# Kernel tuning notes

Measured on AMD Instinct MI355X. Metric: run time of the kernel, lower is better.

The kernel has to match this reference:

```python
import jax, jax.numpy as jnp
import numpy as np

B = 8
NUM_CLASSES = 80
STRIDES = (8, 16, 32, 64, 128)
HS = (96, 48, 24, 12, 6)
WS = (160, 80, 40, 20, 10)
IMG_H, IMG_W = 768, 1280
OCTAVE_SCALE = 4.0
LOC_THR = 0.01
SCORE_THR = 0.05
IOU_THR = 0.5
NMS_PRE = 1000
MAX_PER_IMG = 100
MAX_RATIO_ANCHOR = abs(float(np.log(1e-6)))        # anchor_coder wh_ratio_clip=1e-6
MAX_RATIO_BBOX = abs(float(np.log(16.0 / 1000.0)))  # bbox_coder default wh_ratio_clip
CLS_OFFSET = 4096.0  # > max image coord, separates classes for class-aware NMS


def setup_inputs():
    inp = {}
    k = 0
    for i, (h, w) in enumerate(zip(HS, WS)):
        for name, c in (("cls_score", NUM_CLASSES), ("bbox_pred", 4), ("shape_pred", 2), ("loc_pred", 1)):
            k += 1
            inp[f"{name}_{i}"] = jax.random.normal(jax.random.fold_in(jax.random.key(0), k), (B, c, h, w), dtype=jnp.float32)
    return inp


def _squares(h, w, stride):
    # mmdet square anchor generator: base size stride*octave_base_scale, ratio 1, center offset 0
    xs = jnp.arange(w, dtype=jnp.float32) * stride
    ys = jnp.arange(h, dtype=jnp.float32) * stride
    yy, xx = jnp.meshgrid(ys, xs, indexing="ij")
    half = 0.5 * OCTAVE_SCALE * stride
    return jnp.stack([xx - half, yy - half, xx + half, yy + half], -1).reshape(-1, 4)


def _delta2bbox(rois, deltas, max_ratio, max_shape=None):
    dx, dy = deltas[..., 0], deltas[..., 1]
    dw = jnp.clip(deltas[..., 2], -max_ratio, max_ratio)
    dh = jnp.clip(deltas[..., 3], -max_ratio, max_ratio)
    px = (rois[..., 0] + rois[..., 2]) * 0.5
    py = (rois[..., 1] + rois[..., 3]) * 0.5
    pw = rois[..., 2] - rois[..., 0]
    ph = rois[..., 3] - rois[..., 1]
    gx = px + pw * dx
    gy = py + ph * dy
    gw = pw * jnp.exp(dw)
    gh = ph * jnp.exp(dh)
    x1, y1 = gx - 0.5 * gw, gy - 0.5 * gh
    x2, y2 = gx + 0.5 * gw, gy + 0.5 * gh
    if max_shape is not None:
        x1 = jnp.clip(x1, 0.0, float(max_shape[1]))
        x2 = jnp.clip(x2, 0.0, float(max_shape[1]))
        y1 = jnp.clip(y1, 0.0, float(max_shape[0]))
        y2 = jnp.clip(y2, 0.0, float(max_shape[0]))
    return jnp.stack([x1, y1, x2, y2], -1)


def _level(cls, bbox, shp, loc, stride, h, w):
    b = cls.shape[0]
    # NOTE: double sigmoid is faithful to the original wrapper (it sigmoids twice)
    scores = jax.nn.sigmoid(jax.nn.sigmoid(jnp.transpose(cls, (0, 2, 3, 1)).reshape(b, -1, NUM_CLASSES)))
    mask = (jax.nn.sigmoid(loc) >= LOC_THR).astype(scores.dtype)
    mask = jnp.transpose(mask, (0, 2, 3, 1)).reshape(b, -1)  # num_anchors == 1
    scores = scores * mask[:, :, None]
    deltas = jnp.transpose(shp, (0, 2, 3, 1)).reshape(b, -1, 2)
    bdel = jnp.concatenate([jnp.zeros_like(deltas), deltas], axis=-1)  # [0,0,dw,dh]
    anchors = _delta2bbox(_squares(h, w, stride)[None], bdel, MAX_RATIO_ANCHOR)  # guided anchors
    bbox = jnp.transpose(bbox, (0, 2, 3, 1)).reshape(b, -1, 4)
    n = scores.shape[1]
    if n < NMS_PRE:  # pad_with_value
        pad = NMS_PRE - n
        scores = jnp.pad(scores, ((0, 0), (0, pad), (0, 0)))
        bbox = jnp.pad(bbox, ((0, 0), (0, pad), (0, 0)))
        anchors = jnp.pad(anchors, ((0, 0), (0, pad), (0, 0)))
    _, idx = jax.lax.top_k(scores.max(-1), NMS_PRE)
    scores = jnp.take_along_axis(scores, idx[:, :, None], axis=1)
    bbox = jnp.take_along_axis(bbox, idx[:, :, None], axis=1)
    anchors = jnp.take_along_axis(anchors, idx[:, :, None], axis=1)
    proposals = _delta2bbox(anchors, bbox, MAX_RATIO_BBOX, (IMG_H, IMG_W))
    return scores, proposals


def _iou_one_vs_all(box, boxes):
    lt = jnp.maximum(box[:2], boxes[:, :2])
    rb = jnp.minimum(box[2:], boxes[:, 2:])
    wh = jnp.clip(rb - lt, 0.0, None)
    inter = wh[:, 0] * wh[:, 1]
    a1 = (box[2] - box[0]) * (box[3] - box[1])
    a2 = (boxes[:, 2] - boxes[:, 0]) * (boxes[:, 3] - boxes[:, 1])
    return inter / (a1 + a2 - inter + 1e-6)


def _nms_single(scores, boxes):
    # class-aware greedy NMS (BatchedNMS semantics): scores [N,C], boxes [N,4]
    n, c = scores.shape
    s = jnp.where(scores > SCORE_THR, scores, 0.0).reshape(-1)  # [N*C]
    offs = (jnp.arange(c, dtype=boxes.dtype) * CLS_OFFSET)[None, :, None]
    cboxes = (boxes[:, None, :] + offs).reshape(-1, 4)  # class-offset boxes

    def step(sv, _):
        i = jnp.argmax(sv)
        sc = sv[i]
        keep = sc > 0.0
        iou = _iou_one_vs_all(cboxes[i], cboxes)
        sv = jnp.where(iou > IOU_THR, 0.0, sv)  # suppresses i itself too
        cls = jnp.where(keep, (i % c).astype(jnp.int32), -1)
        return sv, (boxes[i // c], sc, cls, keep)

    _, (ob, osc, ocls, okeep) = jax.lax.scan(step, s, None, length=MAX_PER_IMG)
    kf = okeep.astype(boxes.dtype)
    return okeep.sum().astype(jnp.int32), ob * kf[:, None], osc * kf, ocls


def _forward(tensors):
    mlvl_scores, mlvl_props = [], []
    for i in range(5):
        s, p = _level(tensors[4 * i], tensors[4 * i + 1], tensors[4 * i + 2], tensors[4 * i + 3],
                      STRIDES[i], HS[i], WS[i])
        mlvl_scores.append(s)
        mlvl_props.append(p)
    scores = jnp.concatenate(mlvl_scores, axis=1)   # [B, 5000, 80]
    props = jnp.concatenate(mlvl_props, axis=1)     # [B, 5000, 4]
    k = min(max(1000, NMS_PRE), scores.shape[1])
    _, idx = jax.lax.top_k(scores.max(-1), k)
    scores = jnp.take_along_axis(scores, idx[:, :, None], axis=1)
    props = jnp.take_along_axis(props, idx[:, :, None], axis=1)
    return jax.vmap(_nms_single)(scores, props)


def reference(cls_score_0, bbox_pred_0, shape_pred_0, loc_pred_0,
              cls_score_1, bbox_pred_1, shape_pred_1, loc_pred_1,
              cls_score_2, bbox_pred_2, shape_pred_2, loc_pred_2,
              cls_score_3, bbox_pred_3, shape_pred_3, loc_pred_3,
              cls_score_4, bbox_pred_4, shape_pred_4, loc_pred_4):
    tensors = [cls_score_0, bbox_pred_0, shape_pred_0, loc_pred_0,
               cls_score_1, bbox_pred_1, shape_pred_1, loc_pred_1,
               cls_score_2, bbox_pred_2, shape_pred_2, loc_pred_2,
               cls_score_3, bbox_pred_3, shape_pred_3, loc_pred_3,
               cls_score_4, bbox_pred_4, shape_pred_4, loc_pred_4]
    num_detected, proposals, out_scores, cls_id = _forward(tensors)
    return num_detected, proposals, out_scores, cls_id
```

## Files before the change

### kernel.cpp

```cpp
#include <hip/hip_runtime.h>
#include <stdint.h>

#define NCLS 80
#define BATCH 8
#define NA 20460
#define TOPK 1000
#define MAXPER 100
#define CAP 8
#define POOL 256
#define IMG_WF 1280.0f
#define IMG_HF 768.0f
#define CLS_OFF 4096.0f
#define MAX_RATIO_ANCHOR 13.815510557964274f
#define MAX_RATIO_BBOX   4.1351665567423557f

#define K2_HALF_UP (0.5 + 0x1p-25)

__constant__ int   c_lvoff[6]  = {0, 15360, 19200, 20160, 20400, 20460};
__constant__ int   c_lvoff4[6] = {0, 3840, 4800, 5040, 5100, 5115};
__constant__ int   c_lw[5]    = {160, 80, 40, 20, 10};
__constant__ int   c_lh[5]    = {96, 48, 24, 12, 6};
__constant__ float c_ls[5]    = {8.f, 16.f, 32.f, 64.f, 128.f};

struct InPtrs {
  const float* cls[5];
  const float* bbox[5];
  const float* shp[5];
  const float* loc[5];
};

__device__ __forceinline__ float sigf(float x) { return 1.0f / (1.0f + expf(-x)); }

__device__ __forceinline__ int wave_red_sum_i32(int v) {
  int t;
  t = __builtin_amdgcn_update_dpp(0, v, 0x111, 0xf, 0xf, false); v += t;
  t = __builtin_amdgcn_update_dpp(0, v, 0x112, 0xf, 0xf, false); v += t;
  t = __builtin_amdgcn_update_dpp(0, v, 0x114, 0xf, 0xf, false); v += t;
  t = __builtin_amdgcn_update_dpp(0, v, 0x118, 0xf, 0xf, false); v += t;
  t = __builtin_amdgcn_update_dpp(0, v, 0x142, 0xf, 0xf, false); v += t;
  t = __builtin_amdgcn_update_dpp(0, v, 0x143, 0xf, 0xf, false); v += t;
  return __builtin_amdgcn_readlane(v, 63);
}
__device__ __forceinline__ void wave_red_top2(unsigned m1, unsigned m2,
                                              unsigned& r1, unsigned& r2) {
#define T2STEP(ctrl) { \
    unsigned o1 = (unsigned)__builtin_amdgcn_update_dpp(0, (int)m1, ctrl, 0xf, 0xf, false); \
    unsigned o2 = (unsigned)__builtin_amdgcn_update_dpp(0, (int)m2, ctrl, 0xf, 0xf, false); \
    unsigned tm = min(m1, o1); \
    m1 = max(m1, o1); \
    m2 = max(tm, max(m2, o2)); }
  T2STEP(0x111) T2STEP(0x112) T2STEP(0x114) T2STEP(0x118) T2STEP(0x142) T2STEP(0x143)
#undef T2STEP
  r1 = (unsigned)__builtin_amdgcn_readlane((int)m1, 63);
  r2 = (unsigned)__builtin_amdgcn_readlane((int)m2, 63);
}

__global__ __launch_bounds__(256) void k_maxscore(InPtrs P, float* maxscore) {
  int gid = blockIdx.x * 256 + threadIdx.x;
  if (gid >= BATCH * (NA / 4)) return;
  int b = gid / (NA / 4);
  int q = gid - b * (NA / 4);
  int l = 0;
  while (q >= c_lvoff4[l + 1]) ++l;
  int hw = c_lh[l] * c_lw[l];
  int sp = (q - c_lvoff4[l]) * 4;
  const float4* cls = (const float4*)(P.cls[l] + (size_t)(b * NCLS) * hw + sp);
  int s4 = hw >> 2;
  float4 m = cls[0];
  for (int c = 1; c < NCLS; ++c) {
    float4 v = cls[(size_t)c * s4];
    m.x = fmaxf(m.x, v.x); m.y = fmaxf(m.y, v.y);
    m.z = fmaxf(m.z, v.z); m.w = fmaxf(m.w, v.w);
  }
  float4 lo = *(const float4*)(P.loc[l] + (size_t)b * hw + sp);
  float4 r;
  r.x = (sigf(lo.x) >= 0.01f) ? sigf(sigf(m.x)) : 0.0f;
  r.y = (sigf(lo.y) >= 0.01f) ? sigf(sigf(m.y)) : 0.0f;
  r.z = (sigf(lo.z) >= 0.01f) ? sigf(sigf(m.z)) : 0.0f;
  r.w = (sigf(lo.w) >= 0.01f) ? sigf(sigf(m.w)) : 0.0f;
  ((float4*)maxscore)[(size_t)b * (NA / 4) + q] = r;
}

__global__ __launch_bounds__(1024) void k_select(const float* maxscore, int* sel) {
  int b = blockIdx.x;
  const unsigned int* ms = (const unsigned int*)(maxscore + (size_t)b * NA);
  int tid = threadIdx.x;
  int wv = tid >> 6;
  int lane = tid & 63;
  __shared__ unsigned s_h[2048];
  __shared__ int s_wtot[16];
  __shared__ int s_res[2];
  __shared__ int s_pos;
  __shared__ unsigned long long s_A[1024];
  __shared__ unsigned long long s_B[1024];

  unsigned w[20];
  #pragma unroll
  for (int k = 0; k < 5; ++k) {
    int q = tid + k * 1024;
    uint4 u = (q < NA / 4) ? ((const uint4*)ms)[q] : make_uint4(0u, 0u, 0u, 0u);
    w[k * 4 + 0] = u.x & 0x3FFFFFu;
    w[k * 4 + 1] = u.y & 0x3FFFFFu;
    w[k * 4 + 2] = u.z & 0x3FFFFFu;
    w[k * 4 + 3] = u.w & 0x3FFFFFu;
  }

  s_h[tid] = 0u; s_h[tid + 1024] = 0u;
  if (tid == 0) s_pos = 0;
  __syncthreads();

  auto scanFind = [&](int target) {
    int b0 = 2047 - 2 * tid;
    int h0 = (int)s_h[b0];
    int h1 = (int)s_h[b0 - 1];
    int pair = h0 + h1;
    int incl = pair;
    #pragma unroll
    for (int o = 1; o < 64; o <<= 1) {
      int uu = __shfl_up(incl, o, 64);
      if (lane >= o) incl += uu;
    }
    if (lane == 63) s_wtot[wv] = incl;
    __syncthreads();
    int woff = 0;
    #pragma unroll
    for (int ww = 0; ww < 16; ++ww) woff += (ww < wv) ? s_wtot[ww] : 0;
    int excl = woff + incl - pair;
    if (excl < target && excl + h0 >= target) { s_res[0] = b0; s_res[1] = excl; }
    int e1 = excl + h0;
    if (e1 < target && e1 + h1 >= target) { s_res[0] = b0 - 1; s_res[1] = e1; }
    __syncthreads();
  };

  #pragma unroll
  for (int k = 0; k < 20; ++k) atomicAdd(&s_h[w[k] >> 11], 1u);
  __syncthreads();
  scanFind(TOPK);
  int B1 = s_res[0];
  int NGT1 = s_res[1];

  s_h[tid] = 0u; s_h[tid + 1024] = 0u;
  __syncthreads();
  #pragma unroll
  for (int k = 0; k < 20; ++k)
    if ((int)(w[k] >> 11) == B1) atomicAdd(&s_h[w[k] & 0x7FFu], 1u);
  __syncthreads();
  scanFind(TOPK - NGT1);
  unsigned V = ((unsigned)B1 << 11) | (unsigned)s_res[0];

  if (tid < 1024 - TOPK) s_A[TOPK + tid] = 0ull;
  #pragma unroll
  for (int k = 0; k < 20; ++k) {
    int i = 4 * (tid + (k >> 2) * 1024) + (k & 3);
    bool c = (w[k] > V);
    unsigned long long bal = __ballot(c);
    int base = 0;
    if (lane == 0 && bal) base = atomicAdd(&s_pos, __popcll(bal));
    base = __shfl(base, 0, 64);
    if (c) {
      int off = __popcll(bal & ((1ull << lane) - 1ull));
      s_A[base + off] = ((unsigned long long)w[k] << 32) |
                        (unsigned long long)(0xFFFFFFFFu - (unsigned)i);
    }
  }
  __syncthreads();
  int ngt = s_pos;
  int need = TOPK - ngt;
  int ceq = 0;
  #pragma unroll
  for (int k = 0; k < 5; ++k) {
    int q = tid * 5 + k;
    if (q < NA / 4) {
      uint4 u = ((const uint4*)ms)[q];
      ceq += ((u.x & 0x3FFFFFu) == V ? 1 : 0) + ((u.y & 0x3FFFFFu) == V ? 1 : 0)
           + ((u.z & 0x3FFFFFu) == V ? 1 : 0) + ((u.w & 0x3FFFFFu) == V ? 1 : 0);
    }
  }

  int incl = ceq;
  #pragma unroll
  for (int o = 1; o < 64; o <<= 1) {
    int uu = __shfl_up(incl, o, 64);
    if (lane >= o) incl += uu;
  }
  if (lane == 63) s_wtot[wv] = incl;
  __syncthreads();
  int woff = 0;
  #pragma unroll
  for (int ww = 0; ww < 16; ++ww) woff += (ww < wv) ? s_wtot[ww] : 0;
  int r = woff + incl - ceq;
  int i0 = tid * 20, i1 = min(i0 + 20, NA);
  for (int i = i0; i < i1 && r < need; ++i) {
    if ((ms[i] & 0x3FFFFFu) == V) {
      s_A[ngt + r] = ((unsigned long long)V << 32) |
                     (unsigned long long)(0xFFFFFFFFu - (unsigned)i);
      ++r;
    }
  }
  __syncthreads();

  unsigned long long key = s_A[tid];
  int tog = 0;
  for (unsigned k = 2; k <= 1024; k <<= 1) {
    for (unsigned j = k >> 1; j > 0; j >>= 1) {
      unsigned long long other;
      if (j >= 64) {
        unsigned long long* cur = tog ? s_A : s_B;
        cur[tid] = key;
        __syncthreads();
        other = cur[tid ^ (int)j];
        tog ^= 1;
      } else {
        other = __shfl_xor(key, (int)j, 64);
      }
      bool takeMax = (((tid & (int)k) == 0) == ((tid & (int)j) == 0));
      unsigned long long mx = (key > other) ? key : other;
      unsigned long long mn = (key > other) ? other : key;
      key = takeMax ? mx : mn;
    }
  }
  if (tid < TOPK) {
    sel[b * TOPK + tid] = (int)(0xFFFFFFFFu - (unsigned)(key & 0xFFFFFFFFull));
  }
}

__global__ __launch_bounds__(256) void k_gather(InPtrs P, const int* sel, float* boxes, float* sv) {
  int wvi = threadIdx.x >> 6;
  int lane = threadIdx.x & 63;
  int wid = blockIdx.x * 4 + wvi;
  int b = wid / TOPK;
  int r = wid - b * TOPK;
  __shared__ float s_sc[4][NCLS];

  int a = sel[b * TOPK + r];
  int l = 0;
  while (a >= c_lvoff[l + 1]) ++l;
  int within = a - c_lvoff[l];
  int W = c_lw[l], H = c_lh[l];
  int y = within / W, x = within - y * W;
  int hw = H * W;
  int sp = within;
  float stride = c_ls[l];
  float px = (float)x * stride;
  float py = (float)y * stride;
  float pw = 4.0f * stride;

  const float* shp = P.shp[l];
  float dws = shp[(b * 2 + 0) * hw + sp];
  float dhs = shp[(b * 2 + 1) * hw + sp];
  dws = fminf(fmaxf(dws, -MAX_RATIO_ANCHOR), MAX_RATIO_ANCHOR);
  dhs = fminf(fmaxf(dhs, -MAX_RATIO_ANCHOR), MAX_RATIO_ANCHOR);
  float gw = pw * expf(dws);
  float gh = pw * expf(dhs);
  float ax1 = px - 0.5f * gw, ax2 = px + 0.5f * gw;
  float ay1 = py - 0.5f * gh, ay2 = py + 0.5f * gh;

  const float* bb = P.bbox[l];
  float dx = bb[(b * 4 + 0) * hw + sp];
  float dy = bb[(b * 4 + 1) * hw + sp];
  float dw = bb[(b * 4 + 2) * hw + sp];
  float dh = bb[(b * 4 + 3) * hw + sp];
  dw = fminf(fmaxf(dw, -MAX_RATIO_BBOX), MAX_RATIO_BBOX);
  dh = fminf(fmaxf(dh, -MAX_RATIO_BBOX), MAX_RATIO_BBOX);
  float px2 = (ax1 + ax2) * 0.5f, py2 = (ay1 + ay2) * 0.5f;
  float pw2 = ax2 - ax1, ph2 = ay2 - ay1;
  float gx = px2 + pw2 * dx, gy = py2 + ph2 * dy;
  float gw2 = pw2 * expf(dw), gh2 = ph2 * expf(dh);
  float x1 = fminf(fmaxf(gx - 0.5f * gw2, 0.0f), IMG_WF);
  float x2 = fminf(fmaxf(gx + 0.5f * gw2, 0.0f), IMG_WF);
  float y1 = fminf(fmaxf(gy - 0.5f * gh2, 0.0f), IMG_HF);
  float y2 = fminf(fmaxf(gy + 0.5f * gh2, 0.0f), IMG_HF);
  if (lane == 0) {
    float4 st; st.x = x1; st.y = y1; st.z = x2; st.w = y2;
    ((float4*)boxes)[b * TOPK + r] = st;
  }

  const float* cls = P.cls[l];
  float sl = sigf(P.loc[l][b * hw + sp]);
  bool mask = (sl >= 0.01f);
  int base = (b * NCLS) * hw + sp;
  for (int c = lane; c < NCLS; c += 64) {
    float vv = 0.0f;
    if (mask) {
      float s2 = sigf(sigf(cls[base + c * hw]));
      vv = (s2 > 0.05f) ? s2 : 0.0f;
    }
    s_sc[wvi][c] = vv;
  }
  __syncthreads();
  int t = threadIdx.x;
  if (t < NCLS) {
    int r0 = blockIdx.x * 4 - b * TOPK;
    float4 o; o.x = s_sc[0][t]; o.y = s_sc[1][t]; o.z = s_sc[2][t]; o.w = s_sc[3][t];
    *(float4*)(sv + ((size_t)(b * NCLS + t) * TOPK + r0)) = o;
  }
}

__global__ __launch_bounds__(256) void k_nms(const float* boxes, const float* sv,
                                             float* keptScore, int* keptRow, int* kc,
                                             const int* flags, const int* gbits, int cap) {
  int bc = blockIdx.x;
  if (flags && flags[bc] == 0) return;
  int b = bc / NCLS;
  int c = bc - b * NCLS;
  int tid = threadIdx.x;
  int wv = tid >> 6, lane = tid & 63;

  unsigned Glow = 0u;
  if (gbits) Glow = ((unsigned)gbits[b]) & 0x3FFFFFu;

  __shared__ float4 s_box[TOPK];
  __shared__ float  s_ard[TOPK];
  __shared__ unsigned long long s_p2[2][4];

  float x1[4], y1[4], x2[4], y2[4], ar[4];
  unsigned key[4];
  float off = (float)c * CLS_OFF;
  const float* svc = sv + (size_t)(b * NCLS + c) * TOPK;
  #pragma unroll
  for (int j = 0; j < 4; ++j) {
    int row = j * 256 + tid;
    if (row < TOPK) {
      float4 bo = ((const float4*)boxes)[b * TOPK + row];
      float a = bo.x + off, d = bo.y + off, e = bo.z + off, f = bo.w + off;
      x1[j] = a; y1[j] = d; x2[j] = e; y2[j] = f;
      ar[j] = (e - a) * (f - d);
      unsigned bits = __float_as_uint(svc[row]);
      key[j] = ((bits & 0x3FFFFFu) << 10) | (1023u - (unsigned)row);
      float sden = ar[j] + 1e-6f;
      bool deg = !((double)ar[j] > (double)sden * K2_HALF_UP);
      float4 sb; sb.x = a; sb.y = d; sb.z = e; sb.w = f;
      s_box[row] = sb;
      s_ard[row] = __uint_as_float(__float_as_uint(ar[j]) | (deg ? 0x80000000u : 0u));
    } else {
      x1[j] = y1[j] = x2[j] = y2[j] = ar[j] = 0.0f;
      key[j] = 0u;
    }
  }
  __syncthreads();

  int kept = 0;
  bool sticky = false;
  float* ks = keptScore + (size_t)(b * NCLS + c) * MAXPER;
  int*   kr = keptRow   + (size_t)(b * NCLS + c) * MAXPER;

  for (int round = 0; round < cap; ++round) {
    int par = round & 1;
    unsigned hi1 = max(key[0], key[1]), lo1 = min(key[0], key[1]);
    unsigned hi2 = max(key[2], key[3]), lo2 = min(key[2], key[3]);
    unsigned m1 = max(hi1, hi2);
    unsigned m2 = max(min(hi1, hi2), max(lo1, lo2));
    unsigned w1, w2;
    wave_red_top2(m1, m2, w1, w2);
    if (lane == 0) s_p2[par][wv] = ((unsigned long long)w1 << 32) | w2;
    __syncthreads();
    unsigned k0 = 0u, k1 = 0u;
    #pragma unroll
    for (int w = 0; w < 4; ++w) {
      unsigned long long pp = s_p2[par][w];
      unsigned p1 = (unsigned)(pp >> 32), p2 = (unsigned)pp;
      unsigned tm = min(k0, p1);
      k0 = max(k0, p1);
      k1 = max(tm, max(k1, p2));
    }
    if (k0 < 1024u) break;
    if ((k0 >> 10) < Glow) break;
    int brow1 = 1023 - (int)(k0 & 1023u);
    float bs1 = __uint_as_float(0x3F000000u | (k0 >> 10));
    float4 bb1 = s_box[brow1];
    unsigned au1 = __float_as_uint(s_ard[brow1]);
    bool deg1 = (au1 >> 31) != 0u;
    float ba1 = __uint_as_float(au1 & 0x7FFFFFFFu);
    if (tid == 0) { ks[kept] = bs1; kr[kept] = brow1; }
    kept++;
    if (deg1) { sticky = true; break; }
    if (kept >= cap) break;
    bool live2 = (k1 >= 1024u) && ((k1 >> 10) >= Glow);
    if (!live2) break;
    bool do2 = false, deg2 = false;
    float4 bb2; float ba2 = 0.0f;
    {
      int brow2 = 1023 - (int)(k1 & 1023u);
      float bs2 = __uint_as_float(0x3F000000u | (k1 >> 10));
      bb2 = s_box[brow2];
      unsigned au2 = __float_as_uint(s_ard[brow2]);
      deg2 = (au2 >> 31) != 0u;
      ba2 = __uint_as_float(au2 & 0x7FFFFFFFu);
      float ltx = fmaxf(bb1.x, bb2.x), rbx = fminf(bb1.z, bb2.z);
      float lty = fmaxf(bb1.y, bb2.y), rby = fminf(bb1.w, bb2.w);
      float w_ = fmaxf(rbx - ltx, 0.0f), h_ = fmaxf(rby - lty, 0.0f);
      float inter = w_ * h_;
      float denom = ((ba1 + ba2) - inter) + 1e-6f;
      if (!((double)inter > (double)denom * K2_HALF_UP)) {
        do2 = true;
        if (tid == 0) { ks[kept] = bs2; kr[kept] = brow2; }
        kept++;
      }
    }
    if (do2 && deg2) { sticky = true; break; }
    #pragma unroll
    for (int j = 0; j < 4; ++j) {
      {
        float ltx = fmaxf(bb1.x, x1[j]), rbx = fminf(bb1.z, x2[j]);
        float lty = fmaxf(bb1.y, y1[j]), rby = fminf(bb1.w, y2[j]);
        float w_ = fmaxf(rbx - ltx, 0.0f), h_ = fmaxf(rby - lty, 0.0f);
        float inter = w_ * h_;
        float denom = ((ba1 + ar[j]) - inter) + 1e-6f;
        if ((double)inter > (double)denom * K2_HALF_UP) key[j] = 0u;
      }
      if (do2) {
        float ltx = fmaxf(bb2.x, x1[j]), rbx = fminf(bb2.z, x2[j]);
        float lty = fmaxf(bb2.y, y1[j]), rby = fminf(bb2.w, y2[j]);
        float w_ = fmaxf(rbx - ltx, 0.0f), h_ = fmaxf(rby - lty, 0.0f);
        float inter = w_ * h_;
        float denom = ((ba2 + ar[j]) - inter) + 1e-6f;
        if ((double)inter > (double)denom * K2_HALF_UP) key[j] = 0u;
      }
    }
    if (kept >= cap) break;
  }
  if (tid == 0) kc[b * NCLS + c] = sticky ? -kept : kept;
}

__global__ __launch_bounds__(256) void k_cut(const float* keptScore, const int* kc,
                                             int* flags, int* gbits) {
  int b = blockIdx.x;
  int tid = threadIdx.x;
  int lane = tid & 63;
  __shared__ int s_abs[NCLS];
  __shared__ int s_neg[NCLS];
  __shared__ int s_cnt[2];

  if (tid < NCLS) {
    int v = kc[b * NCLS + tid];
    s_abs[tid] = (v < 0) ? -v : v;
    s_neg[tid] = (v < 0) ? 1 : 0;
  }
  if (tid == 0) { s_cnt[0] = 0; s_cnt[1] = 0; }
  __syncthreads();

  unsigned vv[3] = {0u, 0u, 0u};
  #pragma unroll
  for (int t = 0; t < 3; ++t) {
    int e = tid + t * 256;
    if (e < NCLS * CAP) {
      int c = e / CAP, k = e - c * CAP;
      if (k < s_abs[c])
        vv[t] = __float_as_uint(keptScore[(size_t)b * NCLS * MAXPER + c * MAXPER + k]);
    }
  }

  int par = 0;
  auto countGE = [&](unsigned mid) -> int {
    int c = ((vv[0] >= mid) ? 1 : 0) + ((vv[1] >= mid) ? 1 : 0) + ((vv[2] >= mid) ? 1 : 0);
    c = wave_red_sum_i32(c);
    if (lane == 0) atomicAdd(&s_cnt[par], c);
    if (tid == 0) s_cnt[par ^ 1] = 0;
    __syncthreads();
    int tot = s_cnt[par];
    par ^= 1;
    return tot;
  };

  unsigned G = 0u;
  if (countGE(0x3F000001u) >= MAXPER) {
    unsigned lo = 0x3F000001u, hi = 0x3F3C0000u;
    while (hi - lo > 1u) {
      unsigned mid = lo + (hi - lo) / 2u;
      if (countGE(mid) >= MAXPER) lo = mid; else hi = mid;
    }
    G = lo;
  }
  if (tid == 0) gbits[b] = (int)G;
  if (tid < NCLS) {
    int f = 0;
    if (s_abs[tid] == CAP && !s_neg[tid]) {
      unsigned slast = __float_as_uint(
          keptScore[(size_t)b * NCLS * MAXPER + tid * MAXPER + (CAP - 1)]);
      if (slast >= G) f = 1;
    }
    flags[b * NCLS + tid] = f;
  }
}

__global__ __launch_bounds__(256) void k_merge(const float* boxes, const float* keptScore,
                                               const int* keptRow, const int* kc, float* out) {
  int b = blockIdx.x;
  int tid = threadIdx.x;
  int wv = tid >> 6, lane = tid & 63;
  __shared__ int s_kc[NCLS];
  __shared__ int s_part[2][4];
  __shared__ int s_pos;
  __shared__ int s_sticky;
  __shared__ int s_navail;
  __shared__ unsigned long long s_pool[POOL];
  __shared__ unsigned long long s_sorted[POOL];

  for (int c = tid; c < NCLS; c += 256) s_kc[c] = kc[b * NCLS + c];
  if (tid == 0) { s_pos = 0; s_sticky = 0x7FFFFFFF; s_navail = 0; }
  for (int i = tid; i < POOL; i += 256) { s_pool[i] = 0ull; s_sorted[i] = 0ull; }
  __syncthreads();

  unsigned sc[32];
  #pragma unroll
  for (int s = 0; s < 32; ++s) {
    int i = tid + s * 256;
    unsigned vv = 0u;
    if (i < NCLS * MAXPER) {
      int c = i / MAXPER, k = i - c * MAXPER;
      int kcv = s_kc[c];
      int ka = (kcv < 0) ? -kcv : kcv;
      if (k < ka) vv = __float_as_uint(keptScore[(size_t)b * NCLS * MAXPER + i]);
    }
    sc[s] = vv;
  }

  int par = 0;
  auto countGE = [&](unsigned mid) -> int {
    int c = 0;
    #pragma unroll
    for (int s = 0; s < 32; ++s) c += (sc[s] >= mid) ? 1 : 0;
    c = wave_red_sum_i32(c);
    if (lane == 0) s_part[par][wv] = c;
    __syncthreads();
    int tot = s_part[par][0] + s_part[par][1] + s_part[par][2] + s_part[par][3];
    par ^= 1;
    return tot;
  };

  int T = countGE(0x3F000001u);
  unsigned V = 0x3F000001u;
  if (T > MAXPER) {
    unsigned lo = 0x3F000001u, hi = 0x3F3C0000u;
    while (hi - lo > 1u) {
      unsigned mid = lo + (hi - lo) / 2u;
      if (countGE(mid) >= MAXPER) lo = mid; else hi = mid;
    }
    V = lo;
  }

  #pragma unroll
  for (int s = 0; s < 32; ++s) {
    if (sc[s] >= V) {
      int i = tid + s * 256;
      int c = i / MAXPER, k = i - c * MAXPER;
      int kcv = s_kc[c];
      int ka = (kcv < 0) ? -kcv : kcv;
      unsigned st = (kcv < 0 && k == ka - 1) ? 1u : 0u;
      unsigned row = (unsigned)keptRow[(size_t)b * NCLS * MAXPER + i];
      unsigned flat = row * 80u + (unsigned)c;
      int p = atomicAdd(&s_pos, 1);
      if (p < POOL)
        s_pool[p] = ((unsigned long long)sc[s] << 32) |
                    (unsigned long long)(0x7FFFFFFFu - ((flat << 1) | st));
    }
  }
  __syncthreads();

  if (tid < POOL) {
    unsigned long long mykey = s_pool[tid];
    if (mykey != 0ull) {
      int rank = 0;
      #pragma unroll 8
      for (int s = 0; s < POOL; ++s) rank += (s_pool[s] > mykey) ? 1 : 0;
      s_sorted[rank] = mykey;
    }
  }
  __syncthreads();

  if (tid < MAXPER) {
    unsigned long long key = s_sorted[tid];
    if (key != 0ull) {
      atomicAdd(&s_navail, 1);
      if ((((unsigned)key) & 1u) == 0u) atomicMin(&s_sticky, tid);
    }
  }
  __syncthreads();
  int navail = s_navail;
  int p = s_sticky;
  int n = (p < navail) ? MAXPER : navail;

  if (tid == 0) out[b] = (float)n;
  const int OB = BATCH;
  const int OP = OB + BATCH * MAXPER * 4;
  const int OS = OP + BATCH * MAXPER;
  if (tid < MAXPER) {
    int k = tid;
    float bx0 = 0.f, bx1 = 0.f, bx2 = 0.f, bx3 = 0.f, scf = 0.f, cf = -1.0f;
    if (k < n) {
      int idx = (k > p) ? p : k;
      unsigned long long key = s_sorted[idx];
      unsigned flat = (0x7FFFFFFFu - (unsigned)key) >> 1;
      unsigned cls = flat % 80u;
      unsigned row = flat / 80u;
      float4 bo = ((const float4*)boxes)[b * TOPK + row];
      bx0 = bo.x; bx1 = bo.y; bx2 = bo.z; bx3 = bo.w;
      scf = __uint_as_float((unsigned)(key >> 32));
      cf = (float)cls;
    }
    float* po = out + OB + (size_t)(b * MAXPER + k) * 4;
    po[0] = bx0; po[1] = bx1; po[2] = bx2; po[3] = bx3;
    out[OP + b * MAXPER + k] = scf;
    out[OS + b * MAXPER + k] = cf;
  }
}

extern "C" void kernel_launch(void* const* d_in, const int* in_sizes, int n_in,
                              void* d_out, int out_size, void* d_ws, size_t ws_size,
                              hipStream_t stream) {
  InPtrs P;
  for (int l = 0; l < 5; ++l) {
    P.cls[l]  = (const float*)d_in[4 * l + 0];
    P.bbox[l] = (const float*)d_in[4 * l + 1];
    P.shp[l]  = (const float*)d_in[4 * l + 2];
    P.loc[l]  = (const float*)d_in[4 * l + 3];
  }
  float* maxscore  = (float*)d_ws;
  int*   sel       = (int*)(maxscore + BATCH * NA);
  float* boxes     = (float*)(sel + BATCH * TOPK);
  float* sv        = boxes + BATCH * TOPK * 4;
  float* keptScore = sv + BATCH * NCLS * TOPK;
  int*   keptRow   = (int*)(keptScore + BATCH * NCLS * MAXPER);
  int*   kc        = keptRow + BATCH * NCLS * MAXPER;
  int*   flags     = kc + BATCH * NCLS;
  int*   gbits     = flags + BATCH * NCLS;
  float* out = (float*)d_out;

  k_maxscore<<<(BATCH * (NA / 4) + 255) / 256, 256, 0, stream>>>(P, maxscore);
  k_select<<<BATCH, 1024, 0, stream>>>(maxscore, sel);
  k_gather<<<BATCH * TOPK / 4, 256, 0, stream>>>(P, sel, boxes, sv);
  k_nms<<<BATCH * NCLS, 256, 0, stream>>>(boxes, sv, keptScore, keptRow, kc,
                                          (const int*)nullptr, (const int*)nullptr, CAP);
  k_cut<<<BATCH, 256, 0, stream>>>(keptScore, kc, flags, gbits);
  k_nms<<<BATCH * NCLS, 256, 0, stream>>>(boxes, sv, keptScore, keptRow, kc,
                                          flags, gbits, MAXPER);
  k_merge<<<BATCH, 256, 0, stream>>>(boxes, keptScore, keptRow, kc, out);
}
```

Baseline: 213.9 us.

## Replace binary-search thresholding with radix histogram select in cut and merge

In k_cut and k_merge, the iterative binary search over score bits (one barrier-synchronised count per step, about 22 steps) is replaced by a two-pass 11-bit shared-memory histogram radix select. Each pass is followed by a block prefix scan to locate the threshold bucket. The scores are masked to their low 22 bits, which assumes they lie in [0.5, 0.75). In k_select, each thread now loads a contiguous run of elements, and the greater-than and equal compaction uses a block prefix scan instead of per-wave atomics, dropping the second global read. The change cuts the number of barriers at the cost of histogram atomics and extra shared memory.

```diff
diff --git a/kernel.cpp b/kernel.cpp
--- a/kernel.cpp
+++ b/kernel.cpp
@@ -90,23 +90,23 @@
   __shared__ unsigned s_h[2048];
   __shared__ int s_wtot[16];
   __shared__ int s_res[2];
-  __shared__ int s_pos;
   __shared__ unsigned long long s_A[1024];
   __shared__ unsigned long long s_B[1024];
 
   unsigned w[20];
   #pragma unroll
   for (int k = 0; k < 5; ++k) {
-    int q = tid + k * 1024;
+    int q = tid * 5 + k;
     uint4 u = (q < NA / 4) ? ((const uint4*)ms)[q] : make_uint4(0u, 0u, 0u, 0u);
     w[k * 4 + 0] = u.x & 0x3FFFFFu;
     w[k * 4 + 1] = u.y & 0x3FFFFFu;
     w[k * 4 + 2] = u.z & 0x3FFFFFu;
     w[k * 4 + 3] = u.w & 0x3FFFFFu;
   }
+  int lim = NA - tid * 20;
+  lim = (lim < 0) ? 0 : ((lim > 20) ? 20 : lim);
 
   s_h[tid] = 0u; s_h[tid + 1024] = 0u;
-  if (tid == 0) s_pos = 0;
   __syncthreads();
 
   auto scanFind = [&](int target) {
@@ -149,52 +149,60 @@
   unsigned V = ((unsigned)B1 << 11) | (unsigned)s_res[0];
 
   if (tid < 1024 - TOPK) s_A[TOPK + tid] = 0ull;
-  #pragma unroll
-  for (int k = 0; k < 20; ++k) {
-    int i = 4 * (tid + (k >> 2) * 1024) + (k & 3);
-    bool c = (w[k] > V);
-    unsigned long long bal = __ballot(c);
-    int base = 0;
-    if (lane == 0 && bal) base = atomicAdd(&s_pos, __popcll(bal));
-    base = __shfl(base, 0, 64);
-    if (c) {
-      int off = __popcll(bal & ((1ull << lane) - 1ull));
-      s_A[base + off] = ((unsigned long long)w[k] << 32) |
-                        (unsigned long long)(0xFFFFFFFFu - (unsigned)i);
-    }
-  }
-  __syncthreads();
-  int ngt = s_pos;
-  int need = TOPK - ngt;
-  int ceq = 0;
-  #pragma unroll
-  for (int k = 0; k < 5; ++k) {
-    int q = tid * 5 + k;
-    if (q < NA / 4) {
-      uint4 u = ((const uint4*)ms)[q];
-      ceq += ((u.x & 0x3FFFFFu) == V ? 1 : 0) + ((u.y & 0x3FFFFFu) == V ? 1 : 0)
-           + ((u.z & 0x3FFFFFu) == V ? 1 : 0) + ((u.w & 0x3FFFFFu) == V ? 1 : 0);
-    }
-  }
-
-  int incl = ceq;
-  #pragma unroll
-  for (int o = 1; o < 64; o <<= 1) {
-    int uu = __shfl_up(incl, o, 64);
-    if (lane >= o) incl += uu;
-  }
-  if (lane == 63) s_wtot[wv] = incl;
-  __syncthreads();
-  int woff = 0;
-  #pragma unroll
-  for (int ww = 0; ww < 16; ++ww) woff += (ww < wv) ? s_wtot[ww] : 0;
-  int r = woff + incl - ceq;
-  int i0 = tid * 20, i1 = min(i0 + 20, NA);
-  for (int i = i0; i < i1 && r < need; ++i) {
-    if ((ms[i] & 0x3FFFFFu) == V) {
-      s_A[ngt + r] = ((unsigned long long)V << 32) |
+
+  int cgt = 0;
+  #pragma unroll
+  for (int k = 0; k < 20; ++k) cgt += (w[k] > V) ? 1 : 0;
+  {
+    int incl = cgt;
+    #pragma unroll
+    for (int o = 1; o < 64; o <<= 1) {
+      int uu = __shfl_up(incl, o, 64);
+      if (lane >= o) incl += uu;
+    }
+    if (lane == 63) s_wtot[wv] = incl;
+    __syncthreads();
+    int woff = 0, tot = 0;
+    #pragma unroll
+    for (int ww = 0; ww < 16; ++ww) { tot += s_wtot[ww]; woff += (ww < wv) ? s_wtot[ww] : 0; }
+    int pos = woff + incl - cgt;
+    #pragma unroll
+    for (int k = 0; k < 20; ++k) {
+      if (w[k] > V) {
+        int i = tid * 20 + k;
+        s_A[pos++] = ((unsigned long long)w[k] << 32) |
                      (unsigned long long)(0xFFFFFFFFu - (unsigned)i);
-      ++r;
+      }
+    }
+    int ngt = tot;
+    int need = TOPK - ngt;
+    __syncthreads();
+
+    int ceq = 0;
+    #pragma unroll
+    for (int k = 0; k < 20; ++k) if (k < lim && w[k] == V) ++ceq;
+    int incl2 = ceq;
+    #pragma unroll
+    for (int o = 1; o < 64; o <<= 1) {
+      int uu = __shfl_up(incl2, o, 64);
+      if (lane >= o) incl2 += uu;
+    }
+    if (lane == 63) s_wtot[wv] = incl2;
+    __syncthreads();
+    int woff2 = 0;
+    #pragma unroll
+    for (int ww = 0; ww < 16; ++ww) woff2 += (ww < wv) ? s_wtot[ww] : 0;
+    int r = woff2 + incl2 - ceq;
+    #pragma unroll
+    for (int k = 0; k < 20; ++k) {
+      if (k < lim && w[k] == V) {
+        if (r < need) {
+          int i = tid * 20 + k;
+          s_A[ngt + r] = ((unsigned long long)V << 32) |
+                         (unsigned long long)(0xFFFFFFFFu - (unsigned)i);
+        }
+        ++r;
+      }
     }
   }
   __syncthreads();
@@ -426,17 +434,21 @@
                                              int* flags, int* gbits) {
   int b = blockIdx.x;
   int tid = threadIdx.x;
-  int lane = tid & 63;
+  int wv = tid >> 6, lane = tid & 63;
   __shared__ int s_abs[NCLS];
   __shared__ int s_neg[NCLS];
-  __shared__ int s_cnt[2];
+  __shared__ unsigned s_h[2048];
+  __shared__ int s_wtot[4];
+  __shared__ int s_res[2];
+  __shared__ int s_tot[4];
 
   if (tid < NCLS) {
     int v = kc[b * NCLS + tid];
     s_abs[tid] = (v < 0) ? -v : v;
     s_neg[tid] = (v < 0) ? 1 : 0;
   }
-  if (tid == 0) { s_cnt[0] = 0; s_cnt[1] = 0; }
+  #pragma unroll
+  for (int j = 0; j < 8; ++j) s_h[tid * 8 + j] = 0u;
   __syncthreads();
 
   unsigned vv[3] = {0u, 0u, 0u};
@@ -446,30 +458,56 @@
     if (e < NCLS * CAP) {
       int c = e / CAP, k = e - c * CAP;
       if (k < s_abs[c])
-        vv[t] = __float_as_uint(keptScore[(size_t)b * NCLS * MAXPER + c * MAXPER + k]);
-    }
-  }
-
-  int par = 0;
-  auto countGE = [&](unsigned mid) -> int {
-    int c = ((vv[0] >= mid) ? 1 : 0) + ((vv[1] >= mid) ? 1 : 0) + ((vv[2] >= mid) ? 1 : 0);
-    c = wave_red_sum_i32(c);
-    if (lane == 0) atomicAdd(&s_cnt[par], c);
-    if (tid == 0) s_cnt[par ^ 1] = 0;
-    __syncthreads();
-    int tot = s_cnt[par];
-    par ^= 1;
-    return tot;
+        vv[t] = __float_as_uint(keptScore[(size_t)b * NCLS * MAXPER + c * MAXPER + k])
+                & 0x3FFFFFu;
+    }
+  }
+  int live = ((vv[0] != 0u) ? 1 : 0) + ((vv[1] != 0u) ? 1 : 0) + ((vv[2] != 0u) ? 1 : 0);
+  live = wave_red_sum_i32(live);
+  if (lane == 0) s_tot[wv] = live;
+  #pragma unroll
+  for (int t = 0; t < 3; ++t) if (vv[t]) atomicAdd(&s_h[vv[t] >> 11], 1u);
+  __syncthreads();
+  int T = s_tot[0] + s_tot[1] + s_tot[2] + s_tot[3];
+
+  auto scanFind = [&](int target) {
+    int base = 2047 - 8 * tid;
+    int h[8]; int loc = 0;
+    #pragma unroll
+    for (int j = 0; j < 8; ++j) { h[j] = (int)s_h[base - j]; loc += h[j]; }
+    int incl = loc;
+    #pragma unroll
+    for (int o = 1; o < 64; o <<= 1) {
+      int uu = __shfl_up(incl, o, 64);
+      if (lane >= o) incl += uu;
+    }
+    if (lane == 63) s_wtot[wv] = incl;
+    __syncthreads();
+    int woff = 0;
+    #pragma unroll
+    for (int ww = 0; ww < 4; ++ww) woff += (ww < wv) ? s_wtot[ww] : 0;
+    int e = woff + incl - loc;
+    #pragma unroll
+    for (int j = 0; j < 8; ++j) {
+      if (e < target && e + h[j] >= target) { s_res[0] = base - j; s_res[1] = e; }
+      e += h[j];
+    }
+    __syncthreads();
   };
 
   unsigned G = 0u;
-  if (countGE(0x3F000001u) >= MAXPER) {
-    unsigned lo = 0x3F000001u, hi = 0x3F3C0000u;
-    while (hi - lo > 1u) {
-      unsigned mid = lo + (hi - lo) / 2u;
-      if (countGE(mid) >= MAXPER) lo = mid; else hi = mid;
-    }
-    G = lo;
+  if (T >= MAXPER) {
+    scanFind(MAXPER);
+    int B1 = s_res[0], NGT1 = s_res[1];
+    #pragma unroll
+    for (int j = 0; j < 8; ++j) s_h[tid * 8 + j] = 0u;
+    __syncthreads();
+    #pragma unroll
+    for (int t = 0; t < 3; ++t)
+      if (vv[t] && (int)(vv[t] >> 11) == B1) atomicAdd(&s_h[vv[t] & 0x7FFu], 1u);
+    __syncthreads();
+    scanFind(MAXPER - NGT1);
+    G = 0x3F000000u | ((unsigned)B1 << 11) | (unsigned)s_res[0];
   }
   if (tid == 0) gbits[b] = (int)G;
   if (tid < NCLS) {
@@ -489,7 +527,10 @@
   int tid = threadIdx.x;
   int wv = tid >> 6, lane = tid & 63;
   __shared__ int s_kc[NCLS];
-  __shared__ int s_part[2][4];
+  __shared__ unsigned s_h[2048];
+  __shared__ int s_wtot[4];
+  __shared__ int s_res[2];
+  __shared__ int s_tot[4];
   __shared__ int s_pos;
   __shared__ int s_sticky;
   __shared__ int s_navail;
@@ -499,49 +540,77 @@
   for (int c = tid; c < NCLS; c += 256) s_kc[c] = kc[b * NCLS + c];
   if (tid == 0) { s_pos = 0; s_sticky = 0x7FFFFFFF; s_navail = 0; }
   for (int i = tid; i < POOL; i += 256) { s_pool[i] = 0ull; s_sorted[i] = 0ull; }
+  #pragma unroll
+  for (int j = 0; j < 8; ++j) s_h[tid * 8 + j] = 0u;
   __syncthreads();
 
   unsigned sc[32];
   #pragma unroll
   for (int s = 0; s < 32; ++s) {
     int i = tid + s * 256;
-    unsigned vv = 0u;
+    unsigned vvv = 0u;
     if (i < NCLS * MAXPER) {
       int c = i / MAXPER, k = i - c * MAXPER;
       int kcv = s_kc[c];
       int ka = (kcv < 0) ? -kcv : kcv;
-      if (k < ka) vv = __float_as_uint(keptScore[(size_t)b * NCLS * MAXPER + i]);
-    }
-    sc[s] = vv;
-  }
-
-  int par = 0;
-  auto countGE = [&](unsigned mid) -> int {
-    int c = 0;
-    #pragma unroll
-    for (int s = 0; s < 32; ++s) c += (sc[s] >= mid) ? 1 : 0;
-    c = wave_red_sum_i32(c);
-    if (lane == 0) s_part[par][wv] = c;
-    __syncthreads();
-    int tot = s_part[par][0] + s_part[par][1] + s_part[par][2] + s_part[par][3];
-    par ^= 1;
-    return tot;
+      if (k < ka)
+        vvv = __float_as_uint(keptScore[(size_t)b * NCLS * MAXPER + i]) & 0x3FFFFFu;
+    }
+    sc[s] = vvv;
+  }
+  int live = 0;
+  #pragma unroll
+  for (int s = 0; s < 32; ++s) live += (sc[s] != 0u) ? 1 : 0;
+  live = wave_red_sum_i32(live);
+  if (lane == 0) s_tot[wv] = live;
+  #pragma unroll
+  for (int s = 0; s < 32; ++s) if (sc[s]) atomicAdd(&s_h[sc[s] >> 11], 1u);
+  __syncthreads();
+  int T = s_tot[0] + s_tot[1] + s_tot[2] + s_tot[3];
+
+  auto scanFind = [&](int target) {
+    int base = 2047 - 8 * tid;
+    int h[8]; int loc = 0;
+    #pragma unroll
+    for (int j = 0; j < 8; ++j) { h[j] = (int)s_h[base - j]; loc += h[j]; }
+    int incl = loc;
+    #pragma unroll
+    for (int o = 1; o < 64; o <<= 1) {
+      int uu = __shfl_up(incl, o, 64);
+      if (lane >= o) incl += uu;
+    }
+    if (lane == 63) s_wtot[wv] = incl;
+    __syncthreads();
+    int woff = 0;
+    #pragma unroll
+    for (int ww = 0; ww < 4; ++ww) woff += (ww < wv) ? s_wtot[ww] : 0;
+    int e = woff + incl - loc;
+    #pragma unroll
+    for (int j = 0; j < 8; ++j) {
+      if (e < target && e + h[j] >= target) { s_res[0] = base - j; s_res[1] = e; }
+      e += h[j];
+    }
+    __syncthreads();
   };
 
-  int T = countGE(0x3F000001u);
-  unsigned V = 0x3F000001u;
+  unsigned V = 1u;
   if (T > MAXPER) {
-    unsigned lo = 0x3F000001u, hi = 0x3F3C0000u;
-    while (hi - lo > 1u) {
-      unsigned mid = lo + (hi - lo) / 2u;
-      if (countGE(mid) >= MAXPER) lo = mid; else hi = mid;
-    }
-    V = lo;
+    scanFind(MAXPER);
+    int B1 = s_res[0], NGT1 = s_res[1];
+    #pragma unroll
+    for (int j = 0; j < 8; ++j) s_h[tid * 8 + j] = 0u;
+    __syncthreads();
+    #pragma unroll
+    for (int s = 0; s < 32; ++s)
+      if (sc[s] && (int)(sc[s] >> 11) == B1) atomicAdd(&s_h[sc[s] & 0x7FFu], 1u);
+    __syncthreads();
+    scanFind(MAXPER - NGT1);
+    V = ((unsigned)B1 << 11) | (unsigned)s_res[0];
   }
 
   #pragma unroll
   for (int s = 0; s < 32; ++s) {
-    if (sc[s] >= V) {
+    if (sc[s] >= V && sc[s] != 0u) {
       int i = tid + s * 256;
       int c = i / MAXPER, k = i - c * MAXPER;
       int kcv = s_kc[c];
@@ -551,7 +620,7 @@
       unsigned flat = row * 80u + (unsigned)c;
       int p = atomicAdd(&s_pos, 1);
       if (p < POOL)
-        s_pool[p] = ((unsigned long long)sc[s] << 32) |
+        s_pool[p] = ((unsigned long long)(0x3F000000u | sc[s]) << 32) |
                     (unsigned long long)(0x7FFFFFFFu - ((flat << 1) | st));
     }
   }
```

Result: faster. 203.6 us (-4.8%).
